# Optimization experiments

Measured on AMD Instinct MI355X. Metric: run time of the kernel, lower is better.

Reference implementation:

```python
import jax, jax.numpy as jnp
import numpy as np

MEM_SIZE = 500000
FEAT_DIM = 256
BATCH = 128
MARGIN = 1.0


def setup_inputs() -> dict:
    key = jax.random.key(0)
    k1, k2, k3 = jax.random.split(key, 3)
    x = jax.random.normal(k1, (BATCH, FEAT_DIM), dtype=jnp.float32)
    labels = jax.random.randint(k2, (BATCH,), 0, MEM_SIZE)
    Mem = jax.random.normal(k3, (MEM_SIZE, FEAT_DIM), dtype=jnp.float32)
    return {"x": x, "labels": labels, "Mem": Mem, "topk": 1000}


def reference(x, labels, Mem, topk):
    x_sq = jnp.sum(x * x, axis=1, keepdims=True)          # (B, 1)
    m_sq = jnp.sum(Mem * Mem, axis=1)[None, :]            # (1, M)
    distmat = x_sq + m_sq - 2.0 * (x @ Mem.T)             # (B, M)

    # One-hot positive mask from labels (B, M)
    mask = (labels[:, None] == jnp.arange(Mem.shape[0])[None, :]).astype(distmat.dtype)

    # Positive (same-class) distance; clamp matches torch .clamp(1e-12, 1e12)
    dist1 = distmat * mask
    min_loss = jnp.clip(dist1, 1e-12, 1e12).sum(axis=1)   # (B,)

    # Negatives: topk smallest distances (largest=False) via top_k on negated values
    dist2 = distmat * (1.0 - mask)
    neg_small, _ = jax.lax.top_k(-dist2, topk)            # (B, topk)
    max_loss = (-neg_small).sum(axis=1) / (topk - 1)      # (B,)

    loss = jax.nn.relu(min_loss - max_loss + MARGIN)
    return (loss.mean(), min_loss.mean(), max_loss.mean())
```

## Files before the change

### kernel.cpp

```cpp
#include <hip/hip_runtime.h>
#include <hip/hip_bf16.h>
#include <stdint.h>

#define MEMN 500000
#define FEAT 256
#define BATCHN 128
#define SAMP 8192
#define SSTRIDE 61
#define CAP 16384
#define LCAP 28
#define NTILES ((MEMN + 63) / 64)

typedef __bf16 bf16x8 __attribute__((ext_vector_type(8)));
typedef float float4v __attribute__((ext_vector_type(4)));

__device__ __forceinline__ float bf2f(unsigned bits) {
    return __uint_as_float(bits << 16);
}

__device__ __forceinline__ uint4 pack8(const uint4 u0, const uint4 u1) {
    uint4 p;
    p.x = (u0.y & 0xffff0000u) | (u0.x >> 16);
    p.y = (u0.w & 0xffff0000u) | (u0.z >> 16);
    p.z = (u1.y & 0xffff0000u) | (u1.x >> 16);
    p.w = (u1.w & 0xffff0000u) | (u1.z >> 16);
    return p;
}

__global__ void k0_prep(const float* __restrict__ x, float* __restrict__ xsq,
                        unsigned* __restrict__ cnt, float* __restrict__ dpos) {
    int t = threadIdx.x;
    if (t < BATCHN) {
        const float4* row = (const float4*)(x + t * FEAT);
        float s = 0.f;
        for (int i = 0; i < FEAT / 4; i++) {
            float4 v = row[i];
            s += v.x * v.x + v.y * v.y + v.z * v.z + v.w * v.w;
        }
        xsq[t] = s;
        cnt[t] = 0u;
        dpos[t] = 0.f;
    }
}

__global__ void k1_sample(const float* __restrict__ x, const float* __restrict__ Mem,
                          const float* __restrict__ xsq, float* __restrict__ samp) {
    __shared__ ushort mrow[8][FEAT];
    __shared__ float msq[8];
    int t = threadIdx.x;
    int s0 = blockIdx.x * 8;
    {
        int r = t >> 5, c = (t & 31) * 8;
        long mr = (long)(s0 + r) * SSTRIDE;
        const uint4* mp = (const uint4*)(Mem + mr * FEAT + c);
        uint4 u0 = mp[0], u1 = mp[1];
        *(uint4*)(&mrow[r][c]) = pack8(u0, u1);
    }
    __syncthreads();
    if (t < 8) {
        float s = 0.f;
        for (int k = 0; k < FEAT; k++) { float a = bf2f(mrow[t][k]); s += a * a; }
        msq[t] = s;
    }
    __syncthreads();
    for (int q = 0; q < 4; q++) {
        int pair = t + q * 256;
        int sl = pair >> 7, b = pair & 127;
        const float4* xr = (const float4*)(x + b * FEAT);
        float dot = 0.f;
        for (int i = 0; i < FEAT / 8; i++) {
            float4 x0 = xr[2 * i], x1 = xr[2 * i + 1];
            uint4 mv = *(const uint4*)(&mrow[sl][i * 8]);
            unsigned mw[4] = {mv.x, mv.y, mv.z, mv.w};
            float xf[8] = {x0.x, x0.y, x0.z, x0.w, x1.x, x1.y, x1.z, x1.w};
            for (int j = 0; j < 4; j++) {
                dot += xf[2 * j]     * bf2f(mw[j] & 0xffffu)
                     + xf[2 * j + 1] * bf2f(mw[j] >> 16);
            }
        }
        float d = xsq[b] + msq[sl] - 2.f * dot;
        samp[b * SAMP + (s0 + sl)] = d;
    }
}

__global__ void k2_cutoff(const float* __restrict__ samp, float* __restrict__ cutoff) {
    __shared__ unsigned hist[2048];
    __shared__ unsigned part[256];
    int t = threadIdx.x, b = blockIdx.x;
    for (int i = t; i < 2048; i += 256) hist[i] = 0;
    __syncthreads();
    for (int i = t; i < SAMP; i += 256) {
        float d = samp[b * SAMP + i];
        int bin = (int)(d * 2.f);
        bin = bin < 0 ? 0 : (bin > 2047 ? 2047 : bin);
        atomicAdd(&hist[bin], 1u);
    }
    __syncthreads();
    unsigned p = 0;
    for (int j = 0; j < 8; j++) p += hist[t * 8 + j];
    part[t] = p;
    __syncthreads();
    if (t == 0) {
        const unsigned tgt = 98;
        unsigned cum = 0; int binsel = 2047;
        for (int i = 0; i < 256; i++) {
            if (cum + part[i] >= tgt) {
                for (int j = 0; j < 8; j++) {
                    int bb = i * 8 + j;
                    cum += hist[bb];
                    if (cum >= tgt) { binsel = bb; break; }
                }
                break;
            }
            cum += part[i];
        }
        cutoff[b] = (binsel + 1) * 0.5f + 1.0f;
    }
}

__launch_bounds__(256, 2)
__global__ void k3_gemm(const float* __restrict__ x, const float* __restrict__ Mem,
                        const int* __restrict__ labels,
                        const float* __restrict__ xsq, const float* __restrict__ cutoff,
                        unsigned* __restrict__ cnt, float* __restrict__ buf,
                        float* __restrict__ dpos) {
    __shared__ ushort xs[BATCHN * FEAT];
    __shared__ float cbuf[BATCHN * LCAP];
    __shared__ unsigned ccnt[BATCHN];
    int t = threadIdx.x;
    if (t < BATCHN) ccnt[t] = 0u;
    for (int i = 0; i < 16; i++) {
        int c = i * 256 + t;
        int row = c >> 5, cc = c & 31;
        int ccs = cc ^ (row & 7);
        const uint4* xp = (const uint4*)(x + row * FEAT + cc * 8);
        uint4 u0 = xp[0], u1 = xp[1];
        *(uint4*)(&xs[row * FEAT + ccs * 8]) = pack8(u0, u1);
    }
    int lane = t & 63, wave = t >> 6;
    int l15 = lane & 15, quad = lane >> 4;
    int rx = l15 & 7;
    float xsq_v[8], cut_v[8];
    int lab_v[8];
    for (int nt = 0; nt < 8; nt++) {
        int b = nt * 16 + l15;
        xsq_v[nt] = xsq[b];
        cut_v[nt] = cutoff[b];
        lab_v[nt] = labels[b];
    }
    __syncthreads();

    for (int tile = blockIdx.x; tile < NTILES; tile += gridDim.x) {
        int mbase = tile * 64 + wave * 16;
        int m0 = mbase + l15;
        long mA = m0 < MEMN ? m0 : (MEMN - 1);
        const float* aptr = Mem + mA * FEAT + quad * 8;
        uint4 ua[8], ub[8];
#pragma unroll
        for (int ks = 0; ks < 8; ks++) {
            const uint4* ap = (const uint4*)(aptr + ks * 32);
            ua[ks] = ap[0];
            ub[ks] = ap[1];
        }
        float4v acc[8];
#pragma unroll
        for (int nt = 0; nt < 8; nt++) acc[nt] = (float4v){0.f, 0.f, 0.f, 0.f};
        float msqp = 0.f;
#pragma unroll
        for (int ks = 0; ks < 8; ks++) {
            float4 f0 = __builtin_bit_cast(float4, ua[ks]);
            float4 f1 = __builtin_bit_cast(float4, ub[ks]);
            msqp += f0.x * f0.x + f0.y * f0.y + f0.z * f0.z + f0.w * f0.w
                  + f1.x * f1.x + f1.y * f1.y + f1.z * f1.z + f1.w * f1.w;
            uint4 av = pack8(ua[ks], ub[ks]);
            bf16x8 af = __builtin_bit_cast(bf16x8, av);
            int ch = ks * 4 + quad;
#pragma unroll
            for (int nt = 0; nt < 8; nt++) {
                uint4 bv = *(const uint4*)(&xs[(nt * 16 + l15) * FEAT + (ch ^ rx) * 8]);
                bf16x8 bfr = __builtin_bit_cast(bf16x8, bv);
                acc[nt] = __builtin_amdgcn_mfma_f32_16x16x32_bf16(af, bfr, acc[nt], 0, 0, 0);
            }
        }
        float msqf = msqp;
        msqf += __shfl_xor(msqf, 16, 64);
        msqf += __shfl_xor(msqf, 32, 64);
#pragma unroll
        for (int r = 0; r < 4; r++) {
            float msq_r = __shfl(msqf, quad * 4 + r, 64);
            int mg = mbase + quad * 4 + r;
            if (mg < MEMN) {
#pragma unroll
                for (int nt = 0; nt < 8; nt++) {
                    float d = xsq_v[nt] + msq_r - 2.f * acc[nt][r];
                    int b = nt * 16 + l15;
                    if (lab_v[nt] == mg) {
                        dpos[b] = d;
                    } else if (d < cut_v[nt]) {
                        unsigned p = atomicAdd(&ccnt[b], 1u);
                        if (p < LCAP) {
                            cbuf[b * LCAP + p] = d;
                        } else {
                            unsigned q = atomicAdd(&cnt[b], 1u);
                            if (q < CAP) buf[(long)b * CAP + q] = d;
                        }
                    }
                }
            }
        }
    }
    __syncthreads();
    if (t < BATCHN) {
        unsigned nb = ccnt[t];
        if (nb > LCAP) nb = LCAP;
        if (nb) {
            unsigned p = atomicAdd(&cnt[t], nb);
            for (unsigned i = 0; i < nb; i++) {
                unsigned q = p + i;
                if (q < CAP) buf[(long)t * CAP + q] = cbuf[t * LCAP + i];
            }
        }
    }
}

__global__ void k4_select(const float* __restrict__ buf, const unsigned* __restrict__ cnt,
                          const float* __restrict__ cutoff, const float* __restrict__ dpos,
                          const int* __restrict__ topk, float* __restrict__ tri) {
    __shared__ unsigned hist[2048];
    __shared__ unsigned part[256];
    __shared__ float coll[1024];
    __shared__ unsigned ncoll;
    __shared__ int sTb;
    __shared__ unsigned sC1;
    __shared__ float wsum[4];
    int t = threadIdx.x, b = blockIdx.x;
    int k1 = topk[0] - 1;
    unsigned c = cnt[b]; if (c > CAP) c = CAP;
    float invw = 2048.f / cutoff[b];
    for (int i = t; i < 2048; i += 256) hist[i] = 0;
    if (t == 0) ncoll = 0;
    __syncthreads();
    const float* vals = buf + (long)b * CAP;
    for (unsigned i = t; i < c; i += 256) {
        float d = vals[i];
        int bin = (int)(d * invw);
        bin = bin < 0 ? 0 : (bin > 2047 ? 2047 : bin);
        atomicAdd(&hist[bin], 1u);
    }
    __syncthreads();
    unsigned p = 0;
    for (int j = 0; j < 8; j++) p += hist[t * 8 + j];
    part[t] = p;
    __syncthreads();
    if (t == 0) {
        unsigned tgt = (c < (unsigned)k1) ? c : (unsigned)k1;
        unsigned cum = 0; int Tb = 2048; unsigned C1 = 0;
        if (tgt > 0) {
            for (int i = 0; i < 256; i++) {
                if (cum + part[i] >= tgt) {
                    for (int j = 0; j < 8; j++) {
                        int bb = i * 8 + j;
                        if (cum + hist[bb] >= tgt) { Tb = bb; C1 = cum; break; }
                        cum += hist[bb];
                    }
                    break;
                }
                cum += part[i];
            }
        }
        sTb = Tb; sC1 = C1;
    }
    __syncthreads();
    int Tb = sTb; unsigned C1 = sC1;
    float ls = 0.f;
    for (unsigned i = t; i < c; i += 256) {
        float d = vals[i];
        int bin = (int)(d * invw);
        bin = bin < 0 ? 0 : (bin > 2047 ? 2047 : bin);
        if (bin < Tb) ls += d;
        else if (bin == Tb) {
            unsigned ix = atomicAdd(&ncoll, 1u);
            if (ix < 1024) coll[ix] = d;
        }
    }
    ls += __shfl_down(ls, 32, 64); ls += __shfl_down(ls, 16, 64);
    ls += __shfl_down(ls, 8, 64);  ls += __shfl_down(ls, 4, 64);
    ls += __shfl_down(ls, 2, 64);  ls += __shfl_down(ls, 1, 64);
    if ((t & 63) == 0) wsum[t >> 6] = ls;
    __syncthreads();
    if (t == 0) {
        float S = wsum[0] + wsum[1] + wsum[2] + wsum[3];
        unsigned tgt = (c < (unsigned)k1) ? c : (unsigned)k1;
        int r = (int)(tgt - C1);
        unsigned nc = ncoll; if (nc > 1024) nc = 1024;
        for (int i = 0; i < r && i < (int)nc; i++) {
            float mn = 3.4e38f; int mi = 0;
            for (unsigned j = 0; j < nc; j++) if (coll[j] < mn) { mn = coll[j]; mi = (int)j; }
            S += mn; coll[mi] = 3.4e38f;
        }
        float minl = dpos[b];
        minl = minl < 1e-12f ? 1e-12f : (minl > 1e12f ? 1e12f : minl);
        minl += (float)(MEMN - 1) * 1e-12f;
        float maxl = S / (float)k1;
        float loss = minl - maxl + 1.0f; if (loss < 0.f) loss = 0.f;
        tri[b * 3 + 0] = loss; tri[b * 3 + 1] = minl; tri[b * 3 + 2] = maxl;
    }
}

__global__ void k5_final(const float* __restrict__ tri, float* __restrict__ out) {
    __shared__ float ws2[6];
    int t = threadIdx.x;
    float l = tri[t * 3 + 0], mi = tri[t * 3 + 1], mx = tri[t * 3 + 2];
    for (int s = 32; s >= 1; s >>= 1) {
        l += __shfl_down(l, s, 64);
        mi += __shfl_down(mi, s, 64);
        mx += __shfl_down(mx, s, 64);
    }
    if ((t & 63) == 0) { int wv = t >> 6; ws2[wv * 3 + 0] = l; ws2[wv * 3 + 1] = mi; ws2[wv * 3 + 2] = mx; }
    __syncthreads();
    if (t == 0) {
        out[0] = (ws2[0] + ws2[3]) * (1.f / 128.f);
        out[1] = (ws2[1] + ws2[4]) * (1.f / 128.f);
        out[2] = (ws2[2] + ws2[5]) * (1.f / 128.f);
    }
}

__global__ void k_sentinel(float* out) {
    out[0] = -777.f; out[1] = -777.f; out[2] = -777.f;
}

extern "C" void kernel_launch(void* const* d_in, const int* in_sizes, int n_in,
                              void* d_out, int out_size, void* d_ws, size_t ws_size,
                              hipStream_t stream) {
    const float* x     = (const float*)d_in[0];
    const int* labels  = (const int*)d_in[1];
    const float* Mem   = (const float*)d_in[2];
    const int* topk    = (const int*)d_in[3];
    (void)in_sizes; (void)n_in; (void)out_size;

    char* ws = (char*)d_ws;
    const size_t OFF_SAMP = 0;
    const size_t OFF_BUF  = 4194304;
    const size_t OFF_CNT  = OFF_BUF + 8388608;
    const size_t OFF_XSQ  = OFF_CNT + 512;
    const size_t OFF_DPOS = OFF_XSQ + 512;
    const size_t OFF_CUT  = OFF_DPOS + 512;
    const size_t OFF_TRI  = OFF_CUT + 512;
    const size_t NEEDED   = OFF_TRI + 1536;
    if (ws_size < NEEDED) {
        k_sentinel<<<1, 1, 0, stream>>>((float*)d_out);
        return;
    }
    float*    samp   = (float*)(ws + OFF_SAMP);
    float*    buf    = (float*)(ws + OFF_BUF);
    unsigned* cnt    = (unsigned*)(ws + OFF_CNT);
    float*    xsq    = (float*)(ws + OFF_XSQ);
    float*    dpos   = (float*)(ws + OFF_DPOS);
    float*    cutoff = (float*)(ws + OFF_CUT);
    float*    tri    = (float*)(ws + OFF_TRI);

    k0_prep  <<<1,    128, 0, stream>>>(x, xsq, cnt, dpos);
    k1_sample<<<1024, 256, 0, stream>>>(x, Mem, xsq, samp);
    k2_cutoff<<<128,  256, 0, stream>>>(samp, cutoff);
    k3_gemm  <<<2048, 256, 0, stream>>>(x, Mem, labels, xsq, cutoff, cnt, buf, dpos);
    k4_select<<<128,  256, 0, stream>>>(buf, cnt, cutoff, dpos, topk, tri);
    k5_final <<<1,    128, 0, stream>>>(tri, (float*)d_out);
}
```

Baseline: 907.4 us.

## Double-buffer Mem tile loads in register and halve the GEMM grid

The k3 GEMM loop now prefetches the next tile's Mem rows into a second register buffer while computing on the current one, ping-ponging between two 16-entry uint4 buffers. The grid drops from 2048 to 1024 blocks so each block processes more tiles and the prefetch has something to overlap with. k1 also gains a wraparound guard on its sample row index. Extra register pressure from the second buffer under launch_bounds(256,2) could cause spills or lower occupancy, and fewer blocks means less latency hiding from wave parallelism.

```diff
diff --git a/kernel.cpp b/kernel.cpp
--- a/kernel.cpp
+++ b/kernel.cpp
@@ -10,6 +10,7 @@
 #define CAP 16384
 #define LCAP 28
 #define NTILES ((MEMN + 63) / 64)
+#define K3GRID 1024
 
 typedef __bf16 bf16x8 __attribute__((ext_vector_type(8)));
 typedef float float4v __attribute__((ext_vector_type(4)));
@@ -52,6 +53,7 @@
     {
         int r = t >> 5, c = (t & 31) * 8;
         long mr = (long)(s0 + r) * SSTRIDE;
+        if (mr >= MEMN) mr -= MEMN;
         const uint4* mp = (const uint4*)(Mem + mr * FEAT + c);
         uint4 u0 = mp[0], u1 = mp[1];
         *(uint4*)(&mrow[r][c]) = pack8(u0, u1);
@@ -117,6 +119,71 @@
         cutoff[b] = (binsel + 1) * 0.5f + 1.0f;
     }
 }
+
+#define K3_LOAD(P, tileexpr) do {                                              \
+    int mbase_ = (tileexpr) * 64 + wave * 16;                                  \
+    int m0_ = mbase_ + l15;                                                    \
+    long mA_ = m0_ < MEMN ? m0_ : (MEMN - 1);                                  \
+    const uint4* ap_ = (const uint4*)(Mem + mA_ * FEAT + quad * 8);            \
+    _Pragma("unroll")                                                          \
+    for (int ks = 0; ks < 8; ks++) {                                           \
+        P[2 * ks]     = ap_[ks * 8];                                           \
+        P[2 * ks + 1] = ap_[ks * 8 + 1];                                       \
+    }                                                                          \
+} while (0)
+
+#define K3_COMPUTE(P, tileexpr) do {                                           \
+    int mbase_ = (tileexpr) * 64 + wave * 16;                                  \
+    float4v acc_[8];                                                           \
+    _Pragma("unroll")                                                          \
+    for (int nt = 0; nt < 8; nt++) acc_[nt] = (float4v){0.f, 0.f, 0.f, 0.f};   \
+    float msqp_ = 0.f;                                                         \
+    _Pragma("unroll")                                                          \
+    for (int ks = 0; ks < 8; ks++) {                                           \
+        float4 f0_ = __builtin_bit_cast(float4, P[2 * ks]);                    \
+        float4 f1_ = __builtin_bit_cast(float4, P[2 * ks + 1]);                \
+        msqp_ += f0_.x * f0_.x + f0_.y * f0_.y + f0_.z * f0_.z + f0_.w * f0_.w \
+               + f1_.x * f1_.x + f1_.y * f1_.y + f1_.z * f1_.z + f1_.w * f1_.w;\
+        uint4 av_ = pack8(P[2 * ks], P[2 * ks + 1]);                           \
+        bf16x8 af_ = __builtin_bit_cast(bf16x8, av_);                          \
+        int ch_ = ks * 4 + quad;                                               \
+        _Pragma("unroll")                                                      \
+        for (int nt = 0; nt < 8; nt++) {                                       \
+            uint4 bv_ = *(const uint4*)(&xs[(nt * 16 + l15) * FEAT             \
+                                            + (ch_ ^ rx) * 8]);               \
+            bf16x8 bf_ = __builtin_bit_cast(bf16x8, bv_);                      \
+            acc_[nt] = __builtin_amdgcn_mfma_f32_16x16x32_bf16(af_, bf_,       \
+                                                               acc_[nt],       \
+                                                               0, 0, 0);       \
+        }                                                                      \
+    }                                                                          \
+    float msqf_ = msqp_;                                                       \
+    msqf_ += __shfl_xor(msqf_, 16, 64);                                        \
+    msqf_ += __shfl_xor(msqf_, 32, 64);                                        \
+    _Pragma("unroll")                                                          \
+    for (int r = 0; r < 4; r++) {                                              \
+        float msq_r_ = __shfl(msqf_, quad * 4 + r, 64);                        \
+        int mg_ = mbase_ + quad * 4 + r;                                       \
+        if (mg_ < MEMN) {                                                      \
+            _Pragma("unroll")                                                  \
+            for (int nt = 0; nt < 8; nt++) {                                   \
+                float d_ = xsq_v[nt] + msq_r_ - 2.f * acc_[nt][r];             \
+                int b_ = nt * 16 + l15;                                        \
+                if (lab_v[nt] == mg_) {                                        \
+                    dpos[b_] = d_;                                             \
+                } else if (d_ < cut_v[nt]) {                                   \
+                    unsigned p_ = atomicAdd(&ccnt[b_], 1u);                    \
+                    if (p_ < LCAP) {                                           \
+                        cbuf[b_ * LCAP + p_] = d_;                             \
+                    } else {                                                   \
+                        unsigned q_ = atomicAdd(&cnt[b_], 1u);                 \
+                        if (q_ < CAP) buf[(long)b_ * CAP + q_] = d_;           \
+                    }                                                          \
+                }                                                              \
+            }                                                                  \
+        }                                                                      \
+    }                                                                          \
+} while (0)
 
 __launch_bounds__(256, 2)
 __global__ void k3_gemm(const float* __restrict__ x, const float* __restrict__ Mem,
@@ -142,6 +209,7 @@
     int rx = l15 & 7;
     float xsq_v[8], cut_v[8];
     int lab_v[8];
+#pragma unroll
     for (int nt = 0; nt < 8; nt++) {
         int b = nt * 16 + l15;
         xsq_v[nt] = xsq[b];
@@ -150,65 +218,21 @@
     }
     __syncthreads();
 
-    for (int tile = blockIdx.x; tile < NTILES; tile += gridDim.x) {
-        int mbase = tile * 64 + wave * 16;
-        int m0 = mbase + l15;
-        long mA = m0 < MEMN ? m0 : (MEMN - 1);
-        const float* aptr = Mem + mA * FEAT + quad * 8;
-        uint4 ua[8], ub[8];
-#pragma unroll
-        for (int ks = 0; ks < 8; ks++) {
-            const uint4* ap = (const uint4*)(aptr + ks * 32);
-            ua[ks] = ap[0];
-            ub[ks] = ap[1];
-        }
-        float4v acc[8];
-#pragma unroll
-        for (int nt = 0; nt < 8; nt++) acc[nt] = (float4v){0.f, 0.f, 0.f, 0.f};
-        float msqp = 0.f;
-#pragma unroll
-        for (int ks = 0; ks < 8; ks++) {
-            float4 f0 = __builtin_bit_cast(float4, ua[ks]);
-            float4 f1 = __builtin_bit_cast(float4, ub[ks]);
-            msqp += f0.x * f0.x + f0.y * f0.y + f0.z * f0.z + f0.w * f0.w
-                  + f1.x * f1.x + f1.y * f1.y + f1.z * f1.z + f1.w * f1.w;
-            uint4 av = pack8(ua[ks], ub[ks]);
-            bf16x8 af = __builtin_bit_cast(bf16x8, av);
-            int ch = ks * 4 + quad;
-#pragma unroll
-            for (int nt = 0; nt < 8; nt++) {
-                uint4 bv = *(const uint4*)(&xs[(nt * 16 + l15) * FEAT + (ch ^ rx) * 8]);
-                bf16x8 bfr = __builtin_bit_cast(bf16x8, bv);
-                acc[nt] = __builtin_amdgcn_mfma_f32_16x16x32_bf16(af, bfr, acc[nt], 0, 0, 0);
-            }
-        }
-        float msqf = msqp;
-        msqf += __shfl_xor(msqf, 16, 64);
-        msqf += __shfl_xor(msqf, 32, 64);
-#pragma unroll
-        for (int r = 0; r < 4; r++) {
-            float msq_r = __shfl(msqf, quad * 4 + r, 64);
-            int mg = mbase + quad * 4 + r;
-            if (mg < MEMN) {
-#pragma unroll
-                for (int nt = 0; nt < 8; nt++) {
-                    float d = xsq_v[nt] + msq_r - 2.f * acc[nt][r];
-                    int b = nt * 16 + l15;
-                    if (lab_v[nt] == mg) {
-                        dpos[b] = d;
-                    } else if (d < cut_v[nt]) {
-                        unsigned p = atomicAdd(&ccnt[b], 1u);
-                        if (p < LCAP) {
-                            cbuf[b * LCAP + p] = d;
-                        } else {
-                            unsigned q = atomicAdd(&cnt[b], 1u);
-                            if (q < CAP) buf[(long)b * CAP + q] = d;
-                        }
-                    }
-                }
-            }
-        }
-    }
+    uint4 bufA[16], bufB[16];
+    const int G = K3GRID;
+    int t0 = blockIdx.x;
+    if (t0 < NTILES) {
+        K3_LOAD(bufA, t0);
+        for (int tile = t0; tile < NTILES; tile += 2 * G) {
+            int tn1 = tile + G;
+            if (tn1 < NTILES) K3_LOAD(bufB, tn1);
+            K3_COMPUTE(bufA, tile);
+            int tn2 = tile + 2 * G;
+            if (tn2 < NTILES) K3_LOAD(bufA, tn2);
+            if (tn1 < NTILES) K3_COMPUTE(bufB, tn1);
+        }
+    }
+
     __syncthreads();
     if (t < BATCHN) {
         unsigned nb = ccnt[t];
@@ -359,10 +383,10 @@
     float*    cutoff = (float*)(ws + OFF_CUT);
     float*    tri    = (float*)(ws + OFF_TRI);
 
-    k0_prep  <<<1,    128, 0, stream>>>(x, xsq, cnt, dpos);
-    k1_sample<<<1024, 256, 0, stream>>>(x, Mem, xsq, samp);
-    k2_cutoff<<<128,  256, 0, stream>>>(samp, cutoff);
-    k3_gemm  <<<2048, 256, 0, stream>>>(x, Mem, labels, xsq, cutoff, cnt, buf, dpos);
-    k4_select<<<128,  256, 0, stream>>>(buf, cnt, cutoff, dpos, topk, tri);
-    k5_final <<<1,    128, 0, stream>>>(tri, (float*)d_out);
-}
+    k0_prep  <<<1,      128, 0, stream>>>(x, xsq, cnt, dpos);
+    k1_sample<<<1024,   256, 0, stream>>>(x, Mem, xsq, samp);
+    k2_cutoff<<<128,    256, 0, stream>>>(samp, cutoff);
+    k3_gemm  <<<K3GRID, 256, 0, stream>>>(x, Mem, labels, xsq, cutoff, cnt, buf, dpos);
+    k4_select<<<128,    256, 0, stream>>>(buf, cnt, cutoff, dpos, topk, tri);
+    k5_final <<<1,      128, 0, stream>>>(tri, (float*)d_out);
+}
```

New measurement: 1.011 ms. +11.4%, slower.
